# Optimization experiments

Measured on AMD Instinct MI355X. Metric: run time of the kernel, lower is better.

Reference implementation:

```python
import jax, jax.numpy as jnp
import numpy as np

N = 100000   # nodes in batch
E = 1600000  # edges
H = 128      # hidden_channels
G = 500      # number of subgraphs (batch ids)
MAXZ = 1000  # max_z
L = 3        # num_layers


def setup_inputs() -> dict:
    key = jax.random.key(0)
    ks = jax.random.split(key, 12)
    s = 1.0 / np.sqrt(H)
    z = jax.random.randint(ks[0], (N,), 0, MAXZ)
    edge_index = jax.random.randint(ks[1], (2, E), 0, N)
    batch = jnp.repeat(jnp.arange(G), N // G)  # sorted graph ids, 200 nodes/graph
    edge_weight = jax.random.uniform(ks[2], (E,), jnp.float32)
    z_table = jax.random.normal(ks[3], (MAXZ, H), jnp.float32) * s
    conv_Ws = tuple(jax.random.normal(ks[4 + i], (H, H), jnp.float32) * s for i in range(L))
    conv_bs = tuple(jnp.zeros((H,), jnp.float32) for _ in range(L))
    lin1_W = jax.random.normal(ks[8], (H, H), jnp.float32) * s
    lin1_b = jnp.zeros((H,), jnp.float32)
    lin2_W = jax.random.normal(ks[9], (H, 1), jnp.float32) * s
    lin2_b = jnp.zeros((1,), jnp.float32)
    return dict(z=z, edge_index=edge_index, batch=batch, edge_weight=edge_weight,
                z_table=z_table, conv_Ws=conv_Ws, conv_bs=conv_bs,
                lin1_W=lin1_W, lin1_b=lin1_b, lin2_W=lin2_W, lin2_b=lin2_b)


def gcn_norm(edge_index, edge_weight, n):
    # add self loops (fill value 1) and symmetric normalization, as in PyG gcn_norm
    loop = jnp.arange(n)
    row = jnp.concatenate([edge_index[0], loop])
    col = jnp.concatenate([edge_index[1], loop])
    w = jnp.concatenate([edge_weight, jnp.ones((n,), edge_weight.dtype)])
    deg = jax.ops.segment_sum(w, col, num_segments=n)
    dinv = jnp.where(deg > 0, jax.lax.rsqrt(deg), 0.0)
    norm = dinv[row] * w * dinv[col]
    return row, col, norm


def gcn_conv(x, row, col, norm, W, b):
    xw = x @ W                                        # [N,H] GEMM first (PyG order)
    msg = norm[:, None] * xw[row]                     # gather + scale  [E+N, H]
    out = jax.ops.segment_sum(msg, col, num_segments=x.shape[0])  # scatter-add
    return out + b


def reference(z, edge_index, batch, edge_weight, z_table, conv_Ws, conv_bs,
              lin1_W, lin1_b, lin2_W, lin2_b):
    x = z_table[z]                                    # z embedding [N,H]
    row, col, norm = gcn_norm(edge_index, edge_weight, x.shape[0])
    for i in range(L - 1):
        x = jax.nn.relu(gcn_conv(x, row, col, norm, conv_Ws[i], conv_bs[i]))
        # dropout is identity in eval mode
    x = gcn_conv(x, row, col, norm, conv_Ws[-1], conv_bs[-1])
    # first occurrence of each graph id in sorted batch == center node indices
    center = jnp.searchsorted(batch, jnp.arange(G))
    h = x[center] * x[center + 1]                     # src * dst center pair
    h = jax.nn.relu(h @ lin1_W + lin1_b)
    return h @ lin2_W + lin2_b                        # [G,1]
```

## Files before the change

kernel.cpp:

```cpp
#include <hip/hip_runtime.h>
#include <hip/hip_bf16.h>

#define H 128
#define CAP 64
#define GBM 64
#define GBN 64
#define NSWEEP 8
#define CNT_SCALE 16777216.0
#define RSHIFT 17
#define RMASK  0x1FFFF

typedef __attribute__((ext_vector_type(8))) short bf16x8;
typedef __attribute__((ext_vector_type(4))) float f32x4;

__device__ __forceinline__ unsigned short f2b(float f) {
  __hip_bfloat16 h = __float2bfloat16(f);
  union { __hip_bfloat16 h; unsigned short u; } c; c.h = h; return c.u;
}
__device__ __forceinline__ float b2f(unsigned short u) {
  union { unsigned int i; float f; } c; c.i = (unsigned)u << 16; return c.f;
}


__global__ void k_fillb2(const int* __restrict__ row, const int* __restrict__ col,
                         const float* __restrict__ ew, double* __restrict__ dsum,
                         int2* __restrict__ elist, int E, int shift) {
  int e = blockIdx.x * 256 + threadIdx.x;
  if (e >= E) return;
  int c = col[e];
  float w = ew[e];
  if ((c >> shift) != (int)blockIdx.z) return;
  double old = atomicAdd(&dsum[c], (double)w + CNT_SCALE);
  int pos = (int)(old * (1.0 / CNT_SCALE));
  if (pos < CAP) elist[(size_t)c * CAP + pos] = make_int2(row[e], __float_as_int(w));
}

__global__ void k_dinv(const double* __restrict__ dsum, float* __restrict__ dinv,
                       int* __restrict__ cnt, int n) {
  int i = blockIdx.x * 256 + threadIdx.x;
  if (i >= n) return;
  double v = dsum[i];
  double c = floor(v * (1.0 / CNT_SCALE));
  double s = v - c * CNT_SCALE + 1.0;
  dinv[i] = (float)(1.0 / sqrt(s));
  cnt[i] = (int)c;
}

__global__ __launch_bounds__(256) void k_pack(const int* __restrict__ cnt,
    int* __restrict__ cntp, const float* __restrict__ dinv, const int* __restrict__ z,
    int2* __restrict__ elist, int n) {
  int wid = (blockIdx.x * 256 + threadIdx.x) >> 6;
  if (wid >= n) return;
  int lane = threadIdx.x & 63;
  int m = min(cnt[wid], CAP);
  int mp = (m + 7) & ~7;
  if (lane == 0) cntp[wid] = mp;
  float dc = dinv[wid];
  size_t idx = (size_t)wid * CAP + lane;
  if (lane < m) {
    int2 e = elist[idx];
    int r = e.x;
    float nrm = dinv[r] * __int_as_float(e.y) * dc;
    elist[idx] = make_int2(r | (z[r] << RSHIFT), __float_as_int(nrm));
  } else if (lane < mp) {
    elist[idx] = make_int2(0, 0);
  }
}

__global__ void k_wprep(const float* __restrict__ W, unsigned short* __restrict__ whl) {
  int i = blockIdx.x * 256 + threadIdx.x;
  if (i >= H * H) return;
  int k = i >> 7, n = i & 127;
  float w = W[i];
  unsigned short hi = f2b(w);
  whl[n * H + k] = hi;
  whl[H * H + n * H + k] = f2b(w - b2f(hi));
}


__global__ void k_centers(const int* __restrict__ batch, int n, int* __restrict__ clist, int G) {
  int g = blockIdx.x * 256 + threadIdx.x;
  if (g >= G) return;
  int lo = 0, hi = n;
  while (lo < hi) { int mid = (lo + hi) >> 1; if (batch[mid] < g) lo = mid + 1; else hi = mid; }
  clist[2 * g] = lo;
  clist[2 * g + 1] = lo + 1;
}

__global__ __launch_bounds__(256) void k_mark(const int* __restrict__ clist,
    const int2* __restrict__ elist, const int* __restrict__ cnt,
    unsigned int* __restrict__ bitmap, int nc) {
  int widx = (blockIdx.x * 256 + threadIdx.x) >> 6;
  if (widx >= nc) return;
  int lane = threadIdx.x & 63;
  int v = clist[widx];
  if (lane == 0) atomicOr(&bitmap[v >> 5], 1u << (v & 31));
  int m = min(cnt[v], CAP);
  if (lane < m) {
    int r = elist[(size_t)v * CAP + lane].x & RMASK;
    atomicOr(&bitmap[r >> 5], 1u << (r & 31));
  }
}

__global__ void k_compact(const unsigned int* __restrict__ bitmap,
                          int* __restrict__ slist, int* __restrict__ scount, int n) {
  int i = blockIdx.x * 256 + threadIdx.x;
  if (i >= n) return;
  if (bitmap[i >> 5] & (1u << (i & 31))) slist[atomicAdd(scount, 1)] = i;
}


#define FMA4(A, xs, wv) { A[0] = fmaf(xs, wv.x, A[0]); A[1] = fmaf(xs, wv.y, A[1]); \
                          A[2] = fmaf(xs, wv.z, A[2]); A[3] = fmaf(xs, wv.w, A[3]); }

__global__ __launch_bounds__(256, 2) void k_gemm(const float* __restrict__ X,
    const float* __restrict__ Wg, void* __restrict__ Yv, int Nrows,
    const float* __restrict__ bias, int relu, int outbf) {
  __shared__ float Ws[H][GBN + 4];
  int tid = threadIdx.x;
  int bm = blockIdx.x * GBM;
  int bn = blockIdx.y * GBN;
  for (int i = tid; i < H * (GBN / 4); i += 256) {
    int k = i >> 4, c4 = (i & 15) * 4;
    *(float4*)&Ws[k][c4] = *(const float4*)(Wg + k * H + bn + c4);
  }
  __syncthreads();
  int rg = tid >> 4, cg = tid & 15;
  int cg4 = cg * 4;
  int g0 = bm + rg * 4 + 0, g1 = g0 + 1, g2 = g0 + 2, g3 = g0 + 3;
  const float* xp0; const float* xp1; const float* xp2; const float* xp3;
  {
    int c0 = g0 < Nrows ? g0 : Nrows - 1;
    int c1 = g1 < Nrows ? g1 : Nrows - 1;
    int c2 = g2 < Nrows ? g2 : Nrows - 1;
    int c3 = g3 < Nrows ? g3 : Nrows - 1;
    xp0 = X + (size_t)c0 * H; xp1 = X + (size_t)c1 * H;
    xp2 = X + (size_t)c2 * H; xp3 = X + (size_t)c3 * H;
  }
  float a0[4] = {0,0,0,0}, a1[4] = {0,0,0,0}, a2[4] = {0,0,0,0}, a3[4] = {0,0,0,0};
  #pragma unroll 2
  for (int k = 0; k < H; k += 4) {
    float4 x0 = *(const float4*)(xp0 + k);
    float4 x1 = *(const float4*)(xp1 + k);
    float4 x2 = *(const float4*)(xp2 + k);
    float4 x3 = *(const float4*)(xp3 + k);
    float4 w0 = *(const float4*)&Ws[k + 0][cg4];
    float4 w1 = *(const float4*)&Ws[k + 1][cg4];
    float4 w2 = *(const float4*)&Ws[k + 2][cg4];
    float4 w3 = *(const float4*)&Ws[k + 3][cg4];
    FMA4(a0, x0.x, w0) FMA4(a0, x0.y, w1) FMA4(a0, x0.z, w2) FMA4(a0, x0.w, w3)
    FMA4(a1, x1.x, w0) FMA4(a1, x1.y, w1) FMA4(a1, x1.z, w2) FMA4(a1, x1.w, w3)
    FMA4(a2, x2.x, w0) FMA4(a2, x2.y, w1) FMA4(a2, x2.z, w2) FMA4(a2, x2.w, w3)
    FMA4(a3, x3.x, w0) FMA4(a3, x3.y, w1) FMA4(a3, x3.z, w2) FMA4(a3, x3.w, w3)
  }
  if (bias) {
    float4 bb = *(const float4*)(bias + bn + cg4);
    #pragma unroll
    for (int u = 0; u < 4; ++u) {
      a0[u] += ((const float*)&bb)[u]; a1[u] += ((const float*)&bb)[u];
      a2[u] += ((const float*)&bb)[u]; a3[u] += ((const float*)&bb)[u];
    }
  }
  if (relu) {
    #pragma unroll
    for (int u = 0; u < 4; ++u) {
      a0[u] = fmaxf(a0[u], 0.f); a1[u] = fmaxf(a1[u], 0.f);
      a2[u] = fmaxf(a2[u], 0.f); a3[u] = fmaxf(a3[u], 0.f);
    }
  }
  if (outbf) {
    unsigned short* Yb = (unsigned short*)Yv;
    ushort4 h0 = make_ushort4(f2b(a0[0]), f2b(a0[1]), f2b(a0[2]), f2b(a0[3]));
    ushort4 h1 = make_ushort4(f2b(a1[0]), f2b(a1[1]), f2b(a1[2]), f2b(a1[3]));
    ushort4 h2 = make_ushort4(f2b(a2[0]), f2b(a2[1]), f2b(a2[2]), f2b(a2[3]));
    ushort4 h3 = make_ushort4(f2b(a3[0]), f2b(a3[1]), f2b(a3[2]), f2b(a3[3]));
    if (g0 < Nrows) *(ushort4*)(Yb + (size_t)g0 * H + bn + cg4) = h0;
    if (g1 < Nrows) *(ushort4*)(Yb + (size_t)g1 * H + bn + cg4) = h1;
    if (g2 < Nrows) *(ushort4*)(Yb + (size_t)g2 * H + bn + cg4) = h2;
    if (g3 < Nrows) *(ushort4*)(Yb + (size_t)g3 * H + bn + cg4) = h3;
  } else {
    float* Y = (float*)Yv;
    if (g0 < Nrows) *(float4*)(Y + (size_t)g0 * H + bn + cg4) = make_float4(a0[0], a0[1], a0[2], a0[3]);
    if (g1 < Nrows) *(float4*)(Y + (size_t)g1 * H + bn + cg4) = make_float4(a1[0], a1[1], a1[2], a1[3]);
    if (g2 < Nrows) *(float4*)(Y + (size_t)g2 * H + bn + cg4) = make_float4(a2[0], a2[1], a2[2], a2[3]);
    if (g3 < Nrows) *(float4*)(Y + (size_t)g3 * H + bn + cg4) = make_float4(a3[0], a3[1], a3[2], a3[3]);
  }
}


__global__ __launch_bounds__(256, 2) void k_gemm_mfma(const unsigned short* __restrict__ Xb,
    const unsigned short* __restrict__ WHL, unsigned short* __restrict__ Yb, int Nrows) {
  __shared__ unsigned short WsH[H * H];
  __shared__ unsigned short WsL[H * H];
  int tid = threadIdx.x;
  {
    const int4* src = (const int4*)WHL;
    int4* dH = (int4*)WsH;
    int4* dL = (int4*)WsL;
    for (int i = tid; i < 2048; i += 256) {
      dH[i] = src[i];
      dL[i] = src[2048 + i];
    }
  }
  __syncthreads();
  int lane = tid & 63, wave = tid >> 6;
  int mrow = lane & 15, h = lane >> 4;
  int Mbase = blockIdx.x * 64 + wave * 16;
  int arow = Mbase + mrow;
  if (arow >= Nrows) arow = Nrows - 1;
  const unsigned short* xr = Xb + (size_t)arow * H;
  bf16x8 a[4];
  #pragma unroll
  for (int kt = 0; kt < 4; ++kt)
    a[kt] = *(const bf16x8*)(xr + kt * 32 + h * 8);
  f32x4 acc[8];
  #pragma unroll
  for (int nt = 0; nt < 8; ++nt) acc[nt] = (f32x4){0.f, 0.f, 0.f, 0.f};
  #pragma unroll
  for (int nt = 0; nt < 8; ++nt) {
    #pragma unroll
    for (int kt = 0; kt < 4; ++kt) {
      int boff = (nt * 16 + mrow) * H + kt * 32 + h * 8;
      bf16x8 bh = *(const bf16x8*)(WsH + boff);
      bf16x8 bl = *(const bf16x8*)(WsL + boff);
      acc[nt] = __builtin_amdgcn_mfma_f32_16x16x32_bf16(a[kt], bh, acc[nt], 0, 0, 0);
      acc[nt] = __builtin_amdgcn_mfma_f32_16x16x32_bf16(a[kt], bl, acc[nt], 0, 0, 0);
    }
  }
  #pragma unroll
  for (int nt = 0; nt < 8; ++nt) {
    int ocol = nt * 16 + mrow;
    #pragma unroll
    for (int r = 0; r < 4; ++r) {
      int orow = Mbase + 4 * h + r;
      if (orow < Nrows) Yb[(size_t)orow * H + ocol] = f2b(acc[nt][r]);
    }
  }
}


__global__ __launch_bounds__(256) void k_aggb_list(const unsigned short* __restrict__ XWB,
    const int2* __restrict__ elist, const int* __restrict__ cntp,
    const float* __restrict__ dinv, const float* __restrict__ bias,
    float* __restrict__ out, const int* __restrict__ slist,
    const int* __restrict__ scount, int relu) {
  int widx = (blockIdx.x * 256 + threadIdx.x) >> 5;
  if (widx >= *scount) return;
  int wid = slist[widx];
  int c4 = threadIdx.x & 31;
  const ushort4* xw4 = (const ushort4*)XWB;
  int m = cntp[wid];
  const int2* ep = elist + (size_t)wid * CAP;
  float dc = dinv[wid];
  float d2 = dc * dc;
  ushort4 s = xw4[(size_t)wid * 32 + c4];
  float4 acc = make_float4(d2 * b2f(s.x), d2 * b2f(s.y), d2 * b2f(s.z), d2 * b2f(s.w));
  for (int j0 = 0; j0 < m; j0 += 8) {
    int2 Ee[8];
    #pragma unroll
    for (int u = 0; u < 8; ++u) Ee[u] = ep[j0 + u];
    ushort4 V[8];
    #pragma unroll
    for (int u = 0; u < 8; ++u) V[u] = xw4[(size_t)(Ee[u].x & RMASK) * 32 + c4];
    #pragma unroll
    for (int u = 0; u < 8; ++u) {
      float nn = __int_as_float(Ee[u].y);
      acc.x = fmaf(nn, b2f(V[u].x), acc.x);
      acc.y = fmaf(nn, b2f(V[u].y), acc.y);
      acc.z = fmaf(nn, b2f(V[u].z), acc.z);
      acc.w = fmaf(nn, b2f(V[u].w), acc.w);
    }
  }
  float4 bb = ((const float4*)bias)[c4];
  acc.x += bb.x; acc.y += bb.y; acc.z += bb.z; acc.w += bb.w;
  if (relu) {
    acc.x = fmaxf(acc.x, 0.f); acc.y = fmaxf(acc.y, 0.f);
    acc.z = fmaxf(acc.z, 0.f); acc.w = fmaxf(acc.w, 0.f);
  }
  ((float4*)out)[(size_t)wid * 32 + c4] = acc;
}


#define EFMA(nn, vv) { acc.x = fmaf(nn, vv.x, acc.x); acc.y = fmaf(nn, vv.y, acc.y); \
                       acc.z = fmaf(nn, vv.z, acc.z); acc.w = fmaf(nn, vv.w, acc.w); }

__global__ __launch_bounds__(256) void k_agg_last(const float* __restrict__ X,
    const int2* __restrict__ elist, const int* __restrict__ cntp,
    const float* __restrict__ dinv, const int* __restrict__ clist,
    float* __restrict__ out, int nc) {
  int widx = (blockIdx.x * 256 + threadIdx.x) >> 5;
  if (widx >= nc) return;
  int v = clist[widx];
  int c4 = threadIdx.x & 31;
  const float4* x4 = (const float4*)X;
  int m = cntp[v];
  const int2* ep = elist + (size_t)v * CAP;
  float dc = dinv[v];
  float d2 = dc * dc;
  float4 s = x4[(size_t)v * 32 + c4];
  float4 acc = make_float4(d2 * s.x, d2 * s.y, d2 * s.z, d2 * s.w);
  for (int j0 = 0; j0 < m; j0 += 8) {
    int2 Ee[8];
    #pragma unroll
    for (int u = 0; u < 8; ++u) Ee[u] = ep[j0 + u];
    float4 V[8];
    #pragma unroll
    for (int u = 0; u < 8; ++u) V[u] = x4[(size_t)(Ee[u].x & RMASK) * 32 + c4];
    #pragma unroll
    for (int u = 0; u < 8; ++u) {
      float nn = __int_as_float(Ee[u].y);
      EFMA(nn, V[u])
    }
  }
  ((float4*)out)[(size_t)widx * 32 + c4] = acc;
}


__global__ __launch_bounds__(256) void k_agg_emb(const float* __restrict__ ZTW,
    const int* __restrict__ z, const int2* __restrict__ elist, const int* __restrict__ cntp,
    const float* __restrict__ dinv, const float* __restrict__ bias,
    unsigned short* __restrict__ out, int n) {
  int wid = (blockIdx.x * 256 + threadIdx.x) >> 5;
  if (wid >= n) return;
  int c4 = threadIdx.x & 31;
  const float4* zt4 = (const float4*)ZTW;
  int m = cntp[wid];
  const int2* ep = elist + (size_t)wid * CAP;
  float dc = dinv[wid];
  float d2 = dc * dc;
  float4 s = zt4[(size_t)z[wid] * 32 + c4];
  float4 acc = make_float4(d2 * s.x, d2 * s.y, d2 * s.z, d2 * s.w);
  for (int j0 = 0; j0 < m; j0 += 8) {
    int2 Ee[8];
    #pragma unroll
    for (int u = 0; u < 8; ++u) Ee[u] = ep[j0 + u];
    float4 V[8];
    #pragma unroll
    for (int u = 0; u < 8; ++u) V[u] = zt4[(size_t)((unsigned)Ee[u].x >> RSHIFT) * 32 + c4];
    #pragma unroll
    for (int u = 0; u < 8; ++u) {
      float nn = __int_as_float(Ee[u].y);
      EFMA(nn, V[u])
    }
  }
  float4 bb = ((const float4*)bias)[c4];
  ushort4 o = make_ushort4(f2b(fmaxf(acc.x + bb.x, 0.f)),
                           f2b(fmaxf(acc.y + bb.y, 0.f)),
                           f2b(fmaxf(acc.z + bb.z, 0.f)),
                           f2b(fmaxf(acc.w + bb.w, 0.f)));
  ((ushort4*)out)[(size_t)wid * 32 + c4] = o;
}


__global__ __launch_bounds__(128) void k_head_y(const float* __restrict__ Y,
    const float* __restrict__ W1, const float* __restrict__ b1,
    const float* __restrict__ W2, const float* __restrict__ b2,
    float* __restrict__ out, int G) {
  int g = blockIdx.x, t = threadIdx.x;
  __shared__ float hs[H];
  hs[t] = Y[(size_t)(2 * g) * H + t] * Y[(size_t)(2 * g + 1) * H + t];
  __syncthreads();
  float a = b1[t];
  #pragma unroll 8
  for (int k = 0; k < H; ++k) a = fmaf(hs[k], W1[k * H + t], a);
  a = fmaxf(a, 0.f);
  a *= W2[t];
  for (int off = 32; off > 0; off >>= 1) a += __shfl_down(a, off);
  __shared__ float wsum[2];
  if ((t & 63) == 0) wsum[t >> 6] = a;
  __syncthreads();
  if (t == 0) out[g] = wsum[0] + wsum[1] + b2[0];
}


extern "C" void kernel_launch(void* const* d_in, const int* in_sizes, int n_in,
                              void* d_out, int out_size, void* d_ws, size_t ws_size,
                              hipStream_t stream) {
  const int* z     = (const int*)d_in[0];
  const int* eidx  = (const int*)d_in[1];
  const int* batch = (const int*)d_in[2];
  const float* ew  = (const float*)d_in[3];
  const float* ztab= (const float*)d_in[4];
  const float *W0, *W1, *W2, *b0, *b1, *b2, *l1W, *l1b, *l2W, *l2b;
  if (n_in >= 15) {
    W0 = (const float*)d_in[5];  W1 = (const float*)d_in[6];  W2 = (const float*)d_in[7];
    b0 = (const float*)d_in[8];  b1 = (const float*)d_in[9];  b2 = (const float*)d_in[10];
    l1W = (const float*)d_in[11]; l1b = (const float*)d_in[12];
    l2W = (const float*)d_in[13]; l2b = (const float*)d_in[14];
  } else {
    const float* Wss = (const float*)d_in[5];
    W0 = Wss; W1 = Wss + H * H; W2 = Wss + 2 * H * H;
    const float* bs = (const float*)d_in[6];
    b0 = bs; b1 = bs + H; b2 = bs + 2 * H;
    l1W = (const float*)d_in[7]; l1b = (const float*)d_in[8];
    l2W = (const float*)d_in[9]; l2b = (const float*)d_in[10];
  }
  int N = in_sizes[0];
  int E = in_sizes[3];
  int ZTOT = in_sizes[4];
  int MAXZ = ZTOT / H;
  int G = out_size;
  float* fout = (float*)d_out;
  int NC = 2 * G;
  int MAXS = NC * (CAP + 1);

  size_t woff = 0;
  auto alloc = [&](size_t bytes) {
    void* p = (char*)d_ws + woff;
    woff += (bytes + 255) & ~(size_t)255;
    return p;
  };
  unsigned short* h1b   = (unsigned short*)alloc((size_t)N * H * 2);
  unsigned short* xwb   = (unsigned short*)alloc((size_t)N * H * 2);
  float*          bufB  = (float*)alloc((size_t)N * H * 4);
  double*         dsum  = (double*)alloc((size_t)N * 8);
  unsigned int*   bitmap= (unsigned int*)alloc(((size_t)N + 31) / 32 * 4);
  int*            scount= (int*)alloc(4);
  float*          dinv  = (float*)alloc((size_t)N * 4);
  int*            cnt   = (int*)alloc((size_t)N * 4);
  int*            cntp  = (int*)alloc((size_t)N * 4);
  float*          ztw   = (float*)alloc((size_t)ZTOT * 4);
  unsigned short* whl   = (unsigned short*)alloc((size_t)2 * H * H * 2);
  int*            clist = (int*)alloc((size_t)NC * 4);
  int*            slist = (int*)alloc((size_t)MAXS * 4);
  float*          agg2  = (float*)alloc((size_t)NC * H * 4);
  float*          ybuf  = (float*)alloc((size_t)NC * H * 4);
  int2*           elist = (int2*)alloc((size_t)N * CAP * 8);

  const int* erow = eidx;
  const int* ecol = eidx + E;

  size_t zlen = ((size_t)N * 8 + 255 & ~(size_t)255) + ((((size_t)N + 31) / 32 * 4 + 255) & ~(size_t)255) + 256;
  hipMemsetAsync(dsum, 0, zlen, stream);

  int nb = (N + 255) / 256;
  int eb = ((E + 255) / 256 + NSWEEP - 1) / NSWEEP * NSWEEP;
  int wgrid = (N + 3) / 4;
  int hgrid = (N + 7) / 8;

  int shift = 0; while ((NSWEEP << shift) < N) ++shift;

  dim3 fgrid(eb, 1, NSWEEP);
  k_fillb2<<<fgrid, 256, 0, stream>>>(erow, ecol, ew, dsum, elist, E, shift);
  k_dinv<<<nb, 256, 0, stream>>>(dsum, dinv, cnt, N);
  k_pack<<<wgrid, 256, 0, stream>>>(cnt, cntp, dinv, z, elist, N);
  dim3 zgrid((MAXZ + GBM - 1) / GBM, H / GBN);
  k_gemm<<<zgrid, 256, 0, stream>>>(ztab, W0, ztw, MAXZ, nullptr, 0, 0);
  k_wprep<<<(H * H + 255) / 256, 256, 0, stream>>>(W1, whl);
  k_centers<<<(G + 255) / 256, 256, 0, stream>>>(batch, N, clist, G);
  k_mark<<<(NC + 3) / 4, 256, 0, stream>>>(clist, elist, cnt, bitmap, NC);
  k_compact<<<nb, 256, 0, stream>>>(bitmap, slist, scount, N);

  k_agg_emb<<<hgrid, 256, 0, stream>>>(ztw, z, elist, cntp, dinv, b0, h1b, N);
  k_gemm_mfma<<<(N + 63) / 64, 256, 0, stream>>>(h1b, whl, xwb, N);
  k_aggb_list<<<(MAXS + 7) / 8, 256, 0, stream>>>(xwb, elist, cntp, dinv, b1, bufB, slist, scount, 1);
  k_agg_last<<<(NC + 7) / 8, 256, 0, stream>>>(bufB, elist, cntp, dinv, clist, agg2, NC);
  dim3 ygrid((NC + GBM - 1) / GBM, H / GBN);
  k_gemm<<<ygrid, 256, 0, stream>>>(agg2, W2, ybuf, NC, b2, 0, 0);

  k_head_y<<<G, 128, 0, stream>>>(ybuf, l1W, l1b, l2W, l2b, fout, G);
}
```

Baseline: 275.2 us.

## Store z-embedding GEMM output in bf16, fuse centers search into mark, reorder early exit

The precomputed z_table@W0 table is now written as bf16 through a flag on the existing GEMM, and the first aggregation gathers ushort4 instead of float4. This halves gather bytes in the embedding aggregation at the cost of rounding that table to bf16. The separate center binary-search kernel is folded into k_mark, which saves one launch. In k_fillb2 the edge-weight load now happens after the sweep filter, so threads outside the current sweep skip it.

```diff
diff --git a/kernel.cpp b/kernel.cpp
--- a/kernel.cpp
+++ b/kernel.cpp
@@ -28,8 +28,8 @@
   int e = blockIdx.x * 256 + threadIdx.x;
   if (e >= E) return;
   int c = col[e];
+  if ((c >> shift) != (int)blockIdx.z) return;
   float w = ew[e];
-  if ((c >> shift) != (int)blockIdx.z) return;
   double old = atomicAdd(&dsum[c], (double)w + CNT_SCALE);
   int pos = (int)(old * (1.0 / CNT_SCALE));
   if (pos < CAP) elist[(size_t)c * CAP + pos] = make_int2(row[e], __float_as_int(w));
@@ -78,23 +78,20 @@
 }
 
 
-__global__ void k_centers(const int* __restrict__ batch, int n, int* __restrict__ clist, int G) {
-  int g = blockIdx.x * 256 + threadIdx.x;
-  if (g >= G) return;
-  int lo = 0, hi = n;
-  while (lo < hi) { int mid = (lo + hi) >> 1; if (batch[mid] < g) lo = mid + 1; else hi = mid; }
-  clist[2 * g] = lo;
-  clist[2 * g + 1] = lo + 1;
-}
-
-__global__ __launch_bounds__(256) void k_mark(const int* __restrict__ clist,
-    const int2* __restrict__ elist, const int* __restrict__ cnt,
+__global__ __launch_bounds__(256) void k_mark(const int* __restrict__ batch, int n,
+    int* __restrict__ clist, const int2* __restrict__ elist, const int* __restrict__ cnt,
     unsigned int* __restrict__ bitmap, int nc) {
   int widx = (blockIdx.x * 256 + threadIdx.x) >> 6;
   if (widx >= nc) return;
   int lane = threadIdx.x & 63;
-  int v = clist[widx];
-  if (lane == 0) atomicOr(&bitmap[v >> 5], 1u << (v & 31));
+  int g = widx >> 1;
+  int lo = 0, hi = n;
+  while (lo < hi) { int mid = (lo + hi) >> 1; if (batch[mid] < g) lo = mid + 1; else hi = mid; }
+  int v = lo + (widx & 1);
+  if (lane == 0) {
+    clist[widx] = v;
+    atomicOr(&bitmap[v >> 5], 1u << (v & 31));
+  }
   int m = min(cnt[v], CAP);
   if (lane < m) {
     int r = elist[(size_t)v * CAP + lane].x & RMASK;
@@ -316,31 +313,34 @@
 }
 
 
-__global__ __launch_bounds__(256) void k_agg_emb(const float* __restrict__ ZTW,
+__global__ __launch_bounds__(256) void k_agg_emb(const unsigned short* __restrict__ ZTW,
     const int* __restrict__ z, const int2* __restrict__ elist, const int* __restrict__ cntp,
     const float* __restrict__ dinv, const float* __restrict__ bias,
     unsigned short* __restrict__ out, int n) {
   int wid = (blockIdx.x * 256 + threadIdx.x) >> 5;
   if (wid >= n) return;
   int c4 = threadIdx.x & 31;
-  const float4* zt4 = (const float4*)ZTW;
+  const ushort4* zt4 = (const ushort4*)ZTW;
   int m = cntp[wid];
   const int2* ep = elist + (size_t)wid * CAP;
   float dc = dinv[wid];
   float d2 = dc * dc;
-  float4 s = zt4[(size_t)z[wid] * 32 + c4];
-  float4 acc = make_float4(d2 * s.x, d2 * s.y, d2 * s.z, d2 * s.w);
+  ushort4 s = zt4[(size_t)z[wid] * 32 + c4];
+  float4 acc = make_float4(d2 * b2f(s.x), d2 * b2f(s.y), d2 * b2f(s.z), d2 * b2f(s.w));
   for (int j0 = 0; j0 < m; j0 += 8) {
     int2 Ee[8];
     #pragma unroll
     for (int u = 0; u < 8; ++u) Ee[u] = ep[j0 + u];
-    float4 V[8];
+    ushort4 V[8];
     #pragma unroll
     for (int u = 0; u < 8; ++u) V[u] = zt4[(size_t)((unsigned)Ee[u].x >> RSHIFT) * 32 + c4];
     #pragma unroll
     for (int u = 0; u < 8; ++u) {
       float nn = __int_as_float(Ee[u].y);
-      EFMA(nn, V[u])
+      acc.x = fmaf(nn, b2f(V[u].x), acc.x);
+      acc.y = fmaf(nn, b2f(V[u].y), acc.y);
+      acc.z = fmaf(nn, b2f(V[u].z), acc.z);
+      acc.w = fmaf(nn, b2f(V[u].w), acc.w);
     }
   }
   float4 bb = ((const float4*)bias)[c4];
@@ -419,7 +419,7 @@
   float*          dinv  = (float*)alloc((size_t)N * 4);
   int*            cnt   = (int*)alloc((size_t)N * 4);
   int*            cntp  = (int*)alloc((size_t)N * 4);
-  float*          ztw   = (float*)alloc((size_t)ZTOT * 4);
+  unsigned short* ztw   = (unsigned short*)alloc((size_t)ZTOT * 2);
   unsigned short* whl   = (unsigned short*)alloc((size_t)2 * H * H * 2);
   int*            clist = (int*)alloc((size_t)NC * 4);
   int*            slist = (int*)alloc((size_t)MAXS * 4);
@@ -445,10 +445,9 @@
   k_dinv<<<nb, 256, 0, stream>>>(dsum, dinv, cnt, N);
   k_pack<<<wgrid, 256, 0, stream>>>(cnt, cntp, dinv, z, elist, N);
   dim3 zgrid((MAXZ + GBM - 1) / GBM, H / GBN);
-  k_gemm<<<zgrid, 256, 0, stream>>>(ztab, W0, ztw, MAXZ, nullptr, 0, 0);
+  k_gemm<<<zgrid, 256, 0, stream>>>(ztab, W0, ztw, MAXZ, nullptr, 0, 1);
   k_wprep<<<(H * H + 255) / 256, 256, 0, stream>>>(W1, whl);
-  k_centers<<<(G + 255) / 256, 256, 0, stream>>>(batch, N, clist, G);
-  k_mark<<<(NC + 3) / 4, 256, 0, stream>>>(clist, elist, cnt, bitmap, NC);
+  k_mark<<<(NC + 3) / 4, 256, 0, stream>>>(batch, N, clist, elist, cnt, bitmap, NC);
   k_compact<<<nb, 256, 0, stream>>>(bitmap, slist, scount, N);
 
   k_agg_emb<<<hgrid, 256, 0, stream>>>(ztw, z, elist, cntp, dinv, b0, h1b, N);
```

Measured after the change: 271.7 us. About the same (-1.2%).
